# Performance work log

Hardware: AMD Instinct MI355X
Metric: run time of the kernel (lower is better)

Reference implementation:

```python
import jax, jax.numpy as jnp
import numpy as np

V, E, H = 32000, 256, 512
B, L = 32, 128
SOS = 0


def _lstm_cell(x, h, c, w_ih, w_hh, b_ih, b_hh):
    # PyTorch LSTMCell: gates ordered i, f, g, o
    gates = x @ w_ih.T + b_ih + h @ w_hh.T + b_hh  # (B, 4H)
    i, f, g, o = jnp.split(gates, 4, axis=-1)
    c_new = jax.nn.sigmoid(f) * c + jax.nn.sigmoid(i) * jnp.tanh(g)
    h_new = jax.nn.sigmoid(o) * jnp.tanh(c_new)
    return h_new, c_new


def setup_inputs() -> dict:
    key = jax.random.key(0)
    ks = jax.random.split(key, 14)
    s_e, s_h = 1.0 / np.sqrt(H), 1.0 / np.sqrt(H)
    return {
        "cnn_output": jax.random.normal(ks[0], (B, H), jnp.float32),
        "embedding": jax.random.normal(ks[1], (V, E), jnp.float32),
        "w_ih1": jax.random.uniform(ks[2], (4 * H, E), jnp.float32, -s_e, s_e),
        "w_hh1": jax.random.uniform(ks[3], (4 * H, H), jnp.float32, -s_e, s_e),
        "b_ih1": jax.random.uniform(ks[4], (4 * H,), jnp.float32, -s_e, s_e),
        "b_hh1": jax.random.uniform(ks[5], (4 * H,), jnp.float32, -s_e, s_e),
        "w_ih2": jax.random.uniform(ks[6], (4 * H, H), jnp.float32, -s_h, s_h),
        "w_hh2": jax.random.uniform(ks[7], (4 * H, H), jnp.float32, -s_h, s_h),
        "b_ih2": jax.random.uniform(ks[8], (4 * H,), jnp.float32, -s_h, s_h),
        "b_hh2": jax.random.uniform(ks[9], (4 * H,), jnp.float32, -s_h, s_h),
        "w_out": jax.random.uniform(ks[10], (V, H), jnp.float32, -s_h, s_h),
        "b_out": jax.random.uniform(ks[11], (V,), jnp.float32, -s_h, s_h),
        "ground_truth": jax.random.randint(ks[12], (B, L), 0, V, jnp.int64 if jax.config.jax_enable_x64 else jnp.int32),
    }


def reference(cnn_output, embedding, w_ih1, w_hh1, b_ih1, b_hh1,
              w_ih2, w_hh2, b_ih2, b_hh2, w_out, b_out, ground_truth):
    # Train mode, teacher_force = 1.0: input at step t is SOS for t=0 else ground_truth[:, t-1].
    batch = cnn_output.shape[0]
    tokens = jnp.concatenate(
        [jnp.full((batch, 1), SOS, ground_truth.dtype), ground_truth[:, :-1]], axis=1
    ).T  # (L, B)

    h1 = jnp.zeros_like(cnn_output)       # hidden_state = zeros
    c1 = cnn_output                        # cell_state   = cnn_output
    h2 = jnp.zeros_like(cnn_output)       # LSTMCell default zero state
    c2 = jnp.zeros_like(cnn_output)

    def step(carry, tok):
        h1, c1, h2, c2 = carry
        embed = embedding[tok]                                        # (B, E)
        h1, c1 = _lstm_cell(embed, h1, c1, w_ih1, w_hh1, b_ih1, b_hh1)
        h2, c2 = _lstm_cell(h1, h2, c2, w_ih2, w_hh2, b_ih2, b_hh2)
        logits = h2 @ w_out.T + b_out                                 # (B, V)
        logp = jax.nn.log_softmax(logits, axis=1)
        return (h1, c1, h2, c2), logp

    _, logps = jax.lax.scan(step, (h1, c1, h2, c2), tokens)  # (L, B, V)
    return jnp.transpose(logps, (1, 0, 2))  # (B, L, V) raw_pred_seq
```

## Files before the change

kernel.cpp:

```cpp
#include <hip/hip_runtime.h>
#include <hip/hip_bf16.h>
#include <stdint.h>

#define B_ 32
#define L_ 128
#define H_ 512
#define E_ 256
#define V_ 32000
#define G4 2048

typedef __attribute__((ext_vector_type(8))) short short8;
typedef __attribute__((ext_vector_type(4))) float f32x4;

__device__ __forceinline__ short f2bf(float f){
  uint32_t u = __builtin_bit_cast(uint32_t, f);
  u += 0x7FFFu + ((u >> 16) & 1u);
  return (short)(u >> 16);
}
__device__ __forceinline__ short8 ld8f_bf(const float* p){
  const f32x4* q = (const f32x4*)p;
  f32x4 a = q[0], b = q[1];
  short8 r;
  r[0]=f2bf(a[0]); r[1]=f2bf(a[1]); r[2]=f2bf(a[2]); r[3]=f2bf(a[3]);
  r[4]=f2bf(b[0]); r[5]=f2bf(b[1]); r[6]=f2bf(b[2]); r[7]=f2bf(b[3]);
  return r;
}
__device__ __forceinline__ f32x4 mfma16(short8 a, short8 b, f32x4 c){
  return __builtin_amdgcn_mfma_f32_16x16x32_bf16(a, b, c, 0, 0, 0);
}
__device__ __forceinline__ float sigm(float x){
  x = fminf(30.f, fmaxf(-30.f, x));
  return 1.f / (1.f + __expf(-x));
}
__device__ __forceinline__ float tanh_f(float x){
  x = fminf(15.f, fmaxf(-15.f, x));
  float e = __expf(-2.f * x);
  return (1.f - e) / (1.f + e);
}

__global__ void k_init(const float* __restrict__ cnn,
    const float* __restrict__ w_hh1, const float* __restrict__ w_ih2,
    const float* __restrict__ w_hh2,
    short* __restrict__ wb1, short* __restrict__ wb2, short* __restrict__ wb3,
    float* __restrict__ c1, float* __restrict__ c2, short* __restrict__ h1b,
    float* __restrict__ row_sum)
{
  const int stride = gridDim.x * blockDim.x;
  const int tid0 = blockIdx.x * blockDim.x + threadIdx.x;
  for (int i = tid0; i < G4 * H_; i += stride){
    wb1[i] = f2bf(w_hh1[i]); wb2[i] = f2bf(w_ih2[i]); wb3[i] = f2bf(w_hh2[i]);
  }
  for (int i = tid0; i < B_ * H_; i += stride){
    c1[i] = cnn[i]; c2[i] = 0.f; h1b[i] = 0; h1b[B_ * H_ + i] = 0;
  }
  for (int i = tid0; i < B_ * L_; i += stride) row_sum[i] = 0.f;
}

__global__ __launch_bounds__(256) void k_xw1(const int* __restrict__ gt,
    const float* __restrict__ emb, const float* __restrict__ w_ih1,
    const float* __restrict__ b_ih1, const float* __restrict__ b_hh1,
    float* __restrict__ xW1)
{
  const int wave = (blockIdx.x << 2) + (threadIdx.x >> 6);
  const int lane = threadIdx.x & 63, l15 = lane & 15, lg = lane >> 4;
  const int mt = wave >> 5, n0 = (wave & 31) * 64;
  const int r = mt * 16 + l15;
  const int tt = r >> 5, bb = r & 31;
  const int tok = (tt == 0) ? 0 : gt[bb * L_ + tt - 1];
  const float* arow = emb + (size_t)tok * E_ + lg * 8;

  f32x4 acc[4] = {};
  for (int kt = 0; kt < 8; ++kt){
    short8 af = ld8f_bf(arow + kt * 32);
    #pragma unroll
    for (int g = 0; g < 4; ++g){
      const int j = n0 + g * 16 + l15;
      short8 bw = ld8f_bf(w_ih1 + (size_t)j * E_ + kt * 32 + lg * 8);
      acc[g] = mfma16(af, bw, acc[g]);
    }
  }
  #pragma unroll
  for (int g = 0; g < 4; ++g){
    const int j = n0 + g * 16 + l15;
    const float bias = b_ih1[j] + b_hh1[j];
    const int rr = mt * 16 + lg * 4;
    #pragma unroll
    for (int reg = 0; reg < 4; ++reg)
      xW1[(size_t)(rr + reg) * G4 + j] = acc[g][reg] + bias;
  }
}

__global__ __launch_bounds__(256) void k_step(int t,
    const float* __restrict__ xW1,
    const short* __restrict__ wb1, const short* __restrict__ wb2,
    const short* __restrict__ wb3,
    const float* __restrict__ b_ih2, const float* __restrict__ b_hh2,
    short* __restrict__ h1b, float* __restrict__ c1, float* __restrict__ c2,
    short* __restrict__ h2all)
{
  __shared__ f32x4 red[3 * 512];
  const int bid = blockIdx.x;
  const int w = threadIdx.x >> 6;
  const int lane = threadIdx.x & 63;
  const int l15 = lane & 15, lg = lane >> 4;

  f32x4 acc[4][2] = {};
  const bool is_l1 = (bid < 32);

  if (is_l1){
    if (t >= L_) return;
    const int u0 = bid * 16;
    const short* h1r = h1b + (size_t)(t & 1) * (B_ * H_);
    const int kbase = w * 128;
    #pragma unroll
    for (int ki = 0; ki < 4; ++ki){
      const int k0 = kbase + ki * 32 + lg * 8;
      short8 a0 = *(const short8*)(h1r + (size_t)l15 * H_ + k0);
      short8 a1 = *(const short8*)(h1r + (size_t)(l15 + 16) * H_ + k0);
      #pragma unroll
      for (int g = 0; g < 4; ++g){
        short8 bw = *(const short8*)(wb1 + (size_t)(g * H_ + u0 + l15) * H_ + k0);
        acc[g][0] = mfma16(a0, bw, acc[g][0]);
        acc[g][1] = mfma16(a1, bw, acc[g][1]);
      }
    }
  } else {
    if (t < 1) return;
    const int s = t - 1;
    const int u0 = (bid - 32) * 16;
    const short* A = nullptr; const short* W = nullptr;
    if (w < 2){ A = h1b + (size_t)(t & 1) * (B_ * H_); W = wb2; }
    else if (s >= 1){ A = h2all + (size_t)(s - 1) * (B_ * H_); W = wb3; }
    if (A){
      const int kbase = (w & 1) * 256;
      #pragma unroll
      for (int ki = 0; ki < 8; ++ki){
        const int k0 = kbase + ki * 32 + lg * 8;
        short8 a0 = *(const short8*)(A + (size_t)l15 * H_ + k0);
        short8 a1 = *(const short8*)(A + (size_t)(l15 + 16) * H_ + k0);
        #pragma unroll
        for (int g = 0; g < 4; ++g){
          short8 bw = *(const short8*)(W + (size_t)(g * H_ + u0 + l15) * H_ + k0);
          acc[g][0] = mfma16(a0, bw, acc[g][0]);
          acc[g][1] = mfma16(a1, bw, acc[g][1]);
        }
      }
    }
  }

  if (w > 0){
    #pragma unroll
    for (int g = 0; g < 4; ++g)
      #pragma unroll
      for (int mt = 0; mt < 2; ++mt)
        red[(w - 1) * 512 + (g * 2 + mt) * 64 + lane] = acc[g][mt];
  }
  __syncthreads();
  if (w != 0) return;
  #pragma unroll
  for (int g = 0; g < 4; ++g)
    #pragma unroll
    for (int mt = 0; mt < 2; ++mt){
      f32x4 v = acc[g][mt];
      v += red[0 * 512 + (g * 2 + mt) * 64 + lane];
      v += red[1 * 512 + (g * 2 + mt) * 64 + lane];
      v += red[2 * 512 + (g * 2 + mt) * 64 + lane];
      acc[g][mt] = v;
    }

  if (is_l1){
    const int u = bid * 16 + l15;
    #pragma unroll
    for (int mt = 0; mt < 2; ++mt)
      #pragma unroll
      for (int reg = 0; reg < 4; ++reg){
        const int bb = mt * 16 + lg * 4 + reg;
        const float* xr = xW1 + (size_t)(t * B_ + bb) * G4;
        float gi = acc[0][mt][reg] + xr[0 * H_ + u];
        float gf = acc[1][mt][reg] + xr[1 * H_ + u];
        float gg = acc[2][mt][reg] + xr[2 * H_ + u];
        float go = acc[3][mt][reg] + xr[3 * H_ + u];
        float co = c1[bb * H_ + u];
        float cn = sigm(gf) * co + sigm(gi) * tanh_f(gg);
        float h  = sigm(go) * tanh_f(cn);
        c1[bb * H_ + u] = cn;
        h1b[(size_t)((t + 1) & 1) * (B_ * H_) + bb * H_ + u] = f2bf(h);
      }
  } else {
    const int s = t - 1;
    const int u = (bid - 32) * 16 + l15;
    float bias[4];
    #pragma unroll
    for (int g = 0; g < 4; ++g) bias[g] = b_ih2[g * H_ + u] + b_hh2[g * H_ + u];
    #pragma unroll
    for (int mt = 0; mt < 2; ++mt)
      #pragma unroll
      for (int reg = 0; reg < 4; ++reg){
        const int bb = mt * 16 + lg * 4 + reg;
        float gi = acc[0][mt][reg] + bias[0];
        float gf = acc[1][mt][reg] + bias[1];
        float gg = acc[2][mt][reg] + bias[2];
        float go = acc[3][mt][reg] + bias[3];
        float co = c2[bb * H_ + u];
        float cn = sigm(gf) * co + sigm(gi) * tanh_f(gg);
        float h  = sigm(go) * tanh_f(cn);
        c2[bb * H_ + u] = cn;
        h2all[(size_t)(s * B_ + bb) * H_ + u] = f2bf(h);
      }
  }
}

__global__ __launch_bounds__(256) void k_gemm_out(
    const short* __restrict__ h2all, const float* __restrict__ w_out,
    const float* __restrict__ b_out, float* __restrict__ out,
    float* __restrict__ row_sum)
{
  __shared__ __align__(16) short As[128 * 40];
  __shared__ __align__(16) short Bs[128 * 40];
  const int r0 = blockIdx.x * 128, n0 = blockIdx.y * 128;
  const int tid = threadIdx.x;
  const int w = tid >> 6, lane = tid & 63, l15 = lane & 15, lg = lane >> 4;
  const int mrow0 = (w >> 1) * 64, ncol0 = (w & 1) * 64;

  f32x4 acc[4][4] = {};

  for (int kt = 0; kt < 16; ++kt){
    const int kg = kt * 32;
    #pragma unroll
    for (int ss = 0; ss < 2; ++ss){
      const int slot = tid + ss * 256;
      const int row = slot >> 2, k8 = (slot & 3) * 8;
      *(short8*)(As + row * 40 + k8) =
          *(const short8*)(h2all + (size_t)(r0 + row) * H_ + kg + k8);
      *(short8*)(Bs + row * 40 + k8) =
          ld8f_bf(w_out + (size_t)(n0 + row) * H_ + kg + k8);
    }
    __syncthreads();
    short8 af[4], bfr[4];
    #pragma unroll
    for (int i = 0; i < 4; ++i){
      af[i]  = *(const short8*)(As + (mrow0 + i * 16 + l15) * 40 + lg * 8);
      bfr[i] = *(const short8*)(Bs + (ncol0 + i * 16 + l15) * 40 + lg * 8);
    }
    #pragma unroll
    for (int mi = 0; mi < 4; ++mi)
      #pragma unroll
      for (int nj = 0; nj < 4; ++nj)
        acc[mi][nj] = mfma16(af[mi], bfr[nj], acc[mi][nj]);
    __syncthreads();
  }

  float bo[4];
  #pragma unroll
  for (int nj = 0; nj < 4; ++nj) bo[nj] = b_out[n0 + ncol0 + nj * 16 + l15];

  #pragma unroll
  for (int mi = 0; mi < 4; ++mi){
    #pragma unroll
    for (int reg = 0; reg < 4; ++reg){
      const int r = r0 + mrow0 + mi * 16 + lg * 4 + reg;
      const int tt = r >> 5, bb = r & 31;
      float* orow = out + ((size_t)bb * L_ + tt) * V_;
      float esum = 0.f;
      #pragma unroll
      for (int nj = 0; nj < 4; ++nj){
        float logit = acc[mi][nj][reg] + bo[nj];
        orow[n0 + ncol0 + nj * 16 + l15] = logit;
        esum += __expf(logit);
      }
      esum += __shfl_xor(esum, 1);
      esum += __shfl_xor(esum, 2);
      esum += __shfl_xor(esum, 4);
      esum += __shfl_xor(esum, 8);
      if (l15 == 0) atomicAdd(&row_sum[r], esum);
    }
  }
}

__global__ void k_lse(float* row_sum){
  int i = blockIdx.x * blockDim.x + threadIdx.x;
  if (i < B_ * L_) row_sum[i] = __logf(row_sum[i]);
}

__global__ void k_fix(float* __restrict__ out, const float* __restrict__ lse){
  const size_t stride = (size_t)gridDim.x * blockDim.x;
  const size_t nvec = (size_t)B_ * L_ * V_ / 4;
  for (size_t i = (size_t)blockIdx.x * blockDim.x + threadIdx.x; i < nvec; i += stride){
    const int orow = (int)(i / (V_ / 4));
    const int tt = orow & (L_ - 1), bb = orow >> 7;
    const float l = lse[tt * B_ + bb];
    f32x4 v = ((const f32x4*)out)[i];
    v[0] -= l; v[1] -= l; v[2] -= l; v[3] -= l;
    ((f32x4*)out)[i] = v;
  }
}

extern "C" void kernel_launch(void* const* d_in, const int* in_sizes, int n_in,
                              void* d_out, int out_size, void* d_ws, size_t ws_size,
                              hipStream_t stream)
{
  (void)in_sizes; (void)n_in; (void)out_size;
  const float* cnn   = (const float*)d_in[0];
  const float* emb   = (const float*)d_in[1];
  const float* w_ih1 = (const float*)d_in[2];
  const float* w_hh1 = (const float*)d_in[3];
  const float* b_ih1 = (const float*)d_in[4];
  const float* b_hh1 = (const float*)d_in[5];
  const float* w_ih2 = (const float*)d_in[6];
  const float* w_hh2 = (const float*)d_in[7];
  const float* b_ih2 = (const float*)d_in[8];
  const float* b_hh2 = (const float*)d_in[9];
  const float* w_out = (const float*)d_in[10];
  const float* b_out = (const float*)d_in[11];
  const int*   gt    = (const int*)d_in[12];
  float* out = (float*)d_out;

  char* p = (char*)d_ws;
  size_t off = 0;
  auto carve = [&](size_t bytes)->char* {
    char* q = p + off; off = (off + bytes + 255) & ~(size_t)255; return q;
  };
  short* wb1     = (short*)carve(2097152);
  short* wb2     = (short*)carve(2097152);
  short* wb3     = (short*)carve(2097152);
  short* h2all   = (short*)carve(4194304);
  short* h1b     = (short*)carve(65536);
  float* c1      = (float*)carve(65536);
  float* c2      = (float*)carve(65536);
  float* row_sum = (float*)carve(16384);
  float* xW1;
  if (ws_size >= off + 33554432ull + 256ull){
    xW1 = (float*)carve(33554432);
  } else {
    xW1 = out;
  }

  hipLaunchKernelGGL(k_init, dim3(1024), dim3(256), 0, stream,
                     cnn, w_hh1, w_ih2, w_hh2, wb1, wb2, wb3, c1, c2, h1b, row_sum);
  hipLaunchKernelGGL(k_xw1, dim3(2048), dim3(256), 0, stream,
                     gt, emb, w_ih1, b_ih1, b_hh1, xW1);
  for (int t = 0; t <= L_; ++t)
    hipLaunchKernelGGL(k_step, dim3(64), dim3(256), 0, stream,
                       t, xW1, wb1, wb2, wb3, b_ih2, b_hh2, h1b, c1, c2, h2all);
  hipLaunchKernelGGL(k_gemm_out, dim3(32, 250), dim3(256), 0, stream,
                     h2all, w_out, b_out, out, row_sum);
  hipLaunchKernelGGL(k_lse, dim3(16), dim3(256), 0, stream, row_sum);
  hipLaunchKernelGGL(k_fix, dim3(2048), dim3(256), 0, stream, out, row_sum);
}
```

Before: 2.399 ms.

## Fuse recurrent steps into persistent cooperative kernel with register-resident weights

Replaces the 129 per-step launches with one cooperative kernel that keeps each block's recurrent weight slices in registers and uses grid.sync between time steps. Cell states now stay in registers, and the h2 layout changes to batch-major so the output GEMM and fix pass index rows directly. The output projection weights are pre-converted to bf16 once, and the GEMM uses a K=64 tile with XOR-swizzled shared memory. The cost is grid-wide barriers and heavy register pressure from holding 32 short8 weight fragments per thread.

```diff
diff --git a/kernel.cpp b/kernel.cpp
--- a/kernel.cpp
+++ b/kernel.cpp
@@ -1,6 +1,9 @@
 #include <hip/hip_runtime.h>
 #include <hip/hip_bf16.h>
+#include <hip/hip_cooperative_groups.h>
 #include <stdint.h>
+
+namespace cg = cooperative_groups;
 
 #define B_ 32
 #define L_ 128
@@ -38,21 +41,16 @@
   return (1.f - e) / (1.f + e);
 }
 
-__global__ void k_init(const float* __restrict__ cnn,
-    const float* __restrict__ w_hh1, const float* __restrict__ w_ih2,
-    const float* __restrict__ w_hh2,
-    short* __restrict__ wb1, short* __restrict__ wb2, short* __restrict__ wb3,
-    float* __restrict__ c1, float* __restrict__ c2, short* __restrict__ h1b,
-    float* __restrict__ row_sum)
+__global__ void k_init(const float* __restrict__ wout, short* __restrict__ wob,
+                       short* __restrict__ h1buf, float* __restrict__ row_sum)
 {
   const int stride = gridDim.x * blockDim.x;
   const int tid0 = blockIdx.x * blockDim.x + threadIdx.x;
-  for (int i = tid0; i < G4 * H_; i += stride){
-    wb1[i] = f2bf(w_hh1[i]); wb2[i] = f2bf(w_ih2[i]); wb3[i] = f2bf(w_hh2[i]);
-  }
-  for (int i = tid0; i < B_ * H_; i += stride){
-    c1[i] = cnn[i]; c2[i] = 0.f; h1b[i] = 0; h1b[B_ * H_ + i] = 0;
-  }
+  if (wob){
+    for (int i = tid0; i < V_ * H_ / 8; i += stride)
+      *(short8*)(wob + (size_t)i * 8) = ld8f_bf(wout + (size_t)i * 8);
+  }
+  for (int i = tid0; i < 2 * B_ * H_; i += stride) h1buf[i] = 0;
   for (int i = tid0; i < B_ * L_; i += stride) row_sum[i] = 0.f;
 }
 
@@ -90,133 +88,128 @@
   }
 }
 
-__global__ __launch_bounds__(256) void k_step(int t,
+__global__ __launch_bounds__(256, 1) void k_rnn(
     const float* __restrict__ xW1,
-    const short* __restrict__ wb1, const short* __restrict__ wb2,
-    const short* __restrict__ wb3,
+    const float* __restrict__ w_hh1, const float* __restrict__ w_ih2,
+    const float* __restrict__ w_hh2,
     const float* __restrict__ b_ih2, const float* __restrict__ b_hh2,
-    short* __restrict__ h1b, float* __restrict__ c1, float* __restrict__ c2,
-    short* __restrict__ h2all)
-{
-  __shared__ f32x4 red[3 * 512];
+    const float* __restrict__ cnn,
+    short* __restrict__ h1buf, short* __restrict__ h2all)
+{
+  __shared__ float gx[4][32][18];
   const int bid = blockIdx.x;
+  const bool isL1 = (bid < 32);
+  const int u0 = (isL1 ? bid : bid - 32) * 16;
   const int w = threadIdx.x >> 6;
   const int lane = threadIdx.x & 63;
   const int l15 = lane & 15, lg = lane >> 4;
-
-  f32x4 acc[4][2] = {};
-  const bool is_l1 = (bid < 32);
-
-  if (is_l1){
-    if (t >= L_) return;
-    const int u0 = bid * 16;
-    const short* h1r = h1b + (size_t)(t & 1) * (B_ * H_);
-    const int kbase = w * 128;
-    #pragma unroll
-    for (int ki = 0; ki < 4; ++ki){
-      const int k0 = kbase + ki * 32 + lg * 8;
-      short8 a0 = *(const short8*)(h1r + (size_t)l15 * H_ + k0);
-      short8 a1 = *(const short8*)(h1r + (size_t)(l15 + 16) * H_ + k0);
-      #pragma unroll
-      for (int g = 0; g < 4; ++g){
-        short8 bw = *(const short8*)(wb1 + (size_t)(g * H_ + u0 + l15) * H_ + k0);
-        acc[g][0] = mfma16(a0, bw, acc[g][0]);
-        acc[g][1] = mfma16(a1, bw, acc[g][1]);
-      }
-    }
+  const int cb = threadIdx.x >> 4;
+  const int cu = threadIdx.x & 15;
+
+  short8 wA[16], wB[16];
+  {
+    const float* W0 = isL1 ? w_hh1 : w_ih2;
+    const float* b0 = W0 + ((size_t)(w * H_ + u0 + l15)) * H_ + lg * 8;
+    #pragma unroll
+    for (int kt = 0; kt < 16; ++kt) wA[kt] = ld8f_bf(b0 + kt * 32);
+    if (!isL1){
+      const float* b1 = w_hh2 + ((size_t)(w * H_ + u0 + l15)) * H_ + lg * 8;
+      #pragma unroll
+      for (int kt = 0; kt < 16; ++kt) wB[kt] = ld8f_bf(b1 + kt * 32);
+    } else {
+      #pragma unroll
+      for (int kt = 0; kt < 16; ++kt) wB[kt] = short8{0,0,0,0,0,0,0,0};
+    }
+  }
+
+  float c_a, c_b, bias2[4];
+  if (isL1){
+    c_a = cnn[cb * H_ + u0 + cu];
+    c_b = cnn[(cb + 16) * H_ + u0 + cu];
+    bias2[0]=bias2[1]=bias2[2]=bias2[3]=0.f;
   } else {
-    if (t < 1) return;
-    const int s = t - 1;
-    const int u0 = (bid - 32) * 16;
-    const short* A = nullptr; const short* W = nullptr;
-    if (w < 2){ A = h1b + (size_t)(t & 1) * (B_ * H_); W = wb2; }
-    else if (s >= 1){ A = h2all + (size_t)(s - 1) * (B_ * H_); W = wb3; }
-    if (A){
-      const int kbase = (w & 1) * 256;
-      #pragma unroll
-      for (int ki = 0; ki < 8; ++ki){
-        const int k0 = kbase + ki * 32 + lg * 8;
-        short8 a0 = *(const short8*)(A + (size_t)l15 * H_ + k0);
-        short8 a1 = *(const short8*)(A + (size_t)(l15 + 16) * H_ + k0);
+    c_a = 0.f; c_b = 0.f;
+    #pragma unroll
+    for (int g = 0; g < 4; ++g)
+      bias2[g] = b_ih2[g * H_ + u0 + cu] + b_hh2[g * H_ + u0 + cu];
+  }
+
+  cg::grid_group grid = cg::this_grid();
+
+  for (int it = 0; it <= L_; ++it){
+    if (isL1 ? (it < L_) : (it >= 1)){
+      const int s = isL1 ? it : it - 1;
+      const short* h1r = h1buf + ((it + 1) & 1) * (B_ * H_);
+      float add_a[4] = {0.f,0.f,0.f,0.f}, add_b[4] = {0.f,0.f,0.f,0.f};
+      if (isL1){
+        const float* xr = xW1 + ((size_t)(s * B_ + cb)) * G4 + u0 + cu;
         #pragma unroll
         for (int g = 0; g < 4; ++g){
-          short8 bw = *(const short8*)(W + (size_t)(g * H_ + u0 + l15) * H_ + k0);
-          acc[g][0] = mfma16(a0, bw, acc[g][0]);
-          acc[g][1] = mfma16(a1, bw, acc[g][1]);
+          add_a[g] = xr[(size_t)g * H_];
+          add_b[g] = xr[(size_t)g * H_ + (size_t)16 * G4];
         }
-      }
-    }
-  }
-
-  if (w > 0){
-    #pragma unroll
-    for (int g = 0; g < 4; ++g)
-      #pragma unroll
-      for (int mt = 0; mt < 2; ++mt)
-        red[(w - 1) * 512 + (g * 2 + mt) * 64 + lane] = acc[g][mt];
-  }
-  __syncthreads();
-  if (w != 0) return;
-  #pragma unroll
-  for (int g = 0; g < 4; ++g)
-    #pragma unroll
-    for (int mt = 0; mt < 2; ++mt){
-      f32x4 v = acc[g][mt];
-      v += red[0 * 512 + (g * 2 + mt) * 64 + lane];
-      v += red[1 * 512 + (g * 2 + mt) * 64 + lane];
-      v += red[2 * 512 + (g * 2 + mt) * 64 + lane];
-      acc[g][mt] = v;
-    }
-
-  if (is_l1){
-    const int u = bid * 16 + l15;
-    #pragma unroll
-    for (int mt = 0; mt < 2; ++mt)
-      #pragma unroll
-      for (int reg = 0; reg < 4; ++reg){
-        const int bb = mt * 16 + lg * 4 + reg;
-        const float* xr = xW1 + (size_t)(t * B_ + bb) * G4;
-        float gi = acc[0][mt][reg] + xr[0 * H_ + u];
-        float gf = acc[1][mt][reg] + xr[1 * H_ + u];
-        float gg = acc[2][mt][reg] + xr[2 * H_ + u];
-        float go = acc[3][mt][reg] + xr[3 * H_ + u];
-        float co = c1[bb * H_ + u];
-        float cn = sigm(gf) * co + sigm(gi) * tanh_f(gg);
-        float h  = sigm(go) * tanh_f(cn);
-        c1[bb * H_ + u] = cn;
-        h1b[(size_t)((t + 1) & 1) * (B_ * H_) + bb * H_ + u] = f2bf(h);
-      }
-  } else {
-    const int s = t - 1;
-    const int u = (bid - 32) * 16 + l15;
-    float bias[4];
-    #pragma unroll
-    for (int g = 0; g < 4; ++g) bias[g] = b_ih2[g * H_ + u] + b_hh2[g * H_ + u];
-    #pragma unroll
-    for (int mt = 0; mt < 2; ++mt)
-      #pragma unroll
-      for (int reg = 0; reg < 4; ++reg){
-        const int bb = mt * 16 + lg * 4 + reg;
-        float gi = acc[0][mt][reg] + bias[0];
-        float gf = acc[1][mt][reg] + bias[1];
-        float gg = acc[2][mt][reg] + bias[2];
-        float go = acc[3][mt][reg] + bias[3];
-        float co = c2[bb * H_ + u];
-        float cn = sigm(gf) * co + sigm(gi) * tanh_f(gg);
-        float h  = sigm(go) * tanh_f(cn);
-        c2[bb * H_ + u] = cn;
-        h2all[(size_t)(s * B_ + bb) * H_ + u] = f2bf(h);
-      }
-  }
-}
-
+      } else {
+        #pragma unroll
+        for (int g = 0; g < 4; ++g){ add_a[g] = bias2[g]; add_b[g] = bias2[g]; }
+      }
+
+      f32x4 acc0 = {0.f,0.f,0.f,0.f}, acc1 = {0.f,0.f,0.f,0.f};
+      #pragma unroll
+      for (int kt = 0; kt < 16; ++kt){
+        const int k0 = kt * 32 + lg * 8;
+        short8 a0 = *(const short8*)(h1r + l15 * H_ + k0);
+        short8 a1 = *(const short8*)(h1r + (l15 + 16) * H_ + k0);
+        acc0 = mfma16(a0, wA[kt], acc0);
+        acc1 = mfma16(a1, wA[kt], acc1);
+      }
+      if (!isL1 && s >= 1){
+        const short* h2r = h2all + (size_t)(s - 1) * H_;
+        #pragma unroll
+        for (int kt = 0; kt < 16; ++kt){
+          const int k0 = kt * 32 + lg * 8;
+          short8 a0 = *(const short8*)(h2r + (size_t)l15 * (L_ * H_) + k0);
+          short8 a1 = *(const short8*)(h2r + (size_t)(l15 + 16) * (L_ * H_) + k0);
+          acc0 = mfma16(a0, wB[kt], acc0);
+          acc1 = mfma16(a1, wB[kt], acc1);
+        }
+      }
+      #pragma unroll
+      for (int r = 0; r < 4; ++r){
+        gx[w][lg * 4 + r][l15]      = acc0[r];
+        gx[w][lg * 4 + r + 16][l15] = acc1[r];
+      }
+      __syncthreads();
+      float ga[4], gb[4];
+      #pragma unroll
+      for (int g = 0; g < 4; ++g){
+        ga[g] = gx[g][cb][cu]      + add_a[g];
+        gb[g] = gx[g][cb + 16][cu] + add_b[g];
+      }
+      c_a = sigm(ga[1]) * c_a + sigm(ga[0]) * tanh_f(ga[2]);
+      float ha = sigm(ga[3]) * tanh_f(c_a);
+      c_b = sigm(gb[1]) * c_b + sigm(gb[0]) * tanh_f(gb[2]);
+      float hb = sigm(gb[3]) * tanh_f(c_b);
+      if (isL1){
+        short* h1w = h1buf + (it & 1) * (B_ * H_);
+        h1w[cb * H_ + u0 + cu]        = f2bf(ha);
+        h1w[(cb + 16) * H_ + u0 + cu] = f2bf(hb);
+      } else {
+        h2all[((size_t)cb * L_ + s) * H_ + u0 + cu]        = f2bf(ha);
+        h2all[((size_t)(cb + 16) * L_ + s) * H_ + u0 + cu] = f2bf(hb);
+      }
+    }
+    grid.sync();
+  }
+}
+
+template<bool PRE>
 __global__ __launch_bounds__(256) void k_gemm_out(
-    const short* __restrict__ h2all, const float* __restrict__ w_out,
-    const float* __restrict__ b_out, float* __restrict__ out,
-    float* __restrict__ row_sum)
-{
-  __shared__ __align__(16) short As[128 * 40];
-  __shared__ __align__(16) short Bs[128 * 40];
+    const short* __restrict__ h2all, const short* __restrict__ wob,
+    const float* __restrict__ wout, const float* __restrict__ b_out,
+    float* __restrict__ out, float* __restrict__ row_sum)
+{
+  __shared__ __align__(16) short As[128 * 64];
+  __shared__ __align__(16) short Bs[128 * 64];
   const int r0 = blockIdx.x * 128, n0 = blockIdx.y * 128;
   const int tid = threadIdx.x;
   const int w = tid >> 6, lane = tid & 63, l15 = lane & 15, lg = lane >> 4;
@@ -224,29 +217,39 @@
 
   f32x4 acc[4][4] = {};
 
-  for (int kt = 0; kt < 16; ++kt){
-    const int kg = kt * 32;
-    #pragma unroll
-    for (int ss = 0; ss < 2; ++ss){
-      const int slot = tid + ss * 256;
-      const int row = slot >> 2, k8 = (slot & 3) * 8;
-      *(short8*)(As + row * 40 + k8) =
-          *(const short8*)(h2all + (size_t)(r0 + row) * H_ + kg + k8);
-      *(short8*)(Bs + row * 40 + k8) =
-          ld8f_bf(w_out + (size_t)(n0 + row) * H_ + kg + k8);
+  for (int kt = 0; kt < 8; ++kt){
+    const int kg = kt * 64;
+    #pragma unroll
+    for (int i = 0; i < 4; ++i){
+      const int id = i * 256 + tid;
+      const int row = id >> 3, c = id & 7;
+      const int cs = c ^ (row & 7);
+      *(short8*)(As + row * 64 + cs * 8) =
+          *(const short8*)(h2all + (size_t)(r0 + row) * H_ + kg + c * 8);
+      if (PRE)
+        *(short8*)(Bs + row * 64 + cs * 8) =
+            *(const short8*)(wob + (size_t)(n0 + row) * H_ + kg + c * 8);
+      else
+        *(short8*)(Bs + row * 64 + cs * 8) =
+            ld8f_bf(wout + (size_t)(n0 + row) * H_ + kg + c * 8);
     }
     __syncthreads();
-    short8 af[4], bfr[4];
-    #pragma unroll
-    for (int i = 0; i < 4; ++i){
-      af[i]  = *(const short8*)(As + (mrow0 + i * 16 + l15) * 40 + lg * 8);
-      bfr[i] = *(const short8*)(Bs + (ncol0 + i * 16 + l15) * 40 + lg * 8);
-    }
-    #pragma unroll
-    for (int mi = 0; mi < 4; ++mi)
-      #pragma unroll
-      for (int nj = 0; nj < 4; ++nj)
-        acc[mi][nj] = mfma16(af[mi], bfr[nj], acc[mi][nj]);
+    #pragma unroll
+    for (int ks = 0; ks < 2; ++ks){
+      short8 af[4], bfr[4];
+      #pragma unroll
+      for (int i = 0; i < 4; ++i){
+        const int ra = mrow0 + i * 16 + l15;
+        af[i]  = *(const short8*)(As + ra * 64 + (((ks * 4 + lg) ^ (ra & 7)) * 8));
+        const int rb = ncol0 + i * 16 + l15;
+        bfr[i] = *(const short8*)(Bs + rb * 64 + (((ks * 4 + lg) ^ (rb & 7)) * 8));
+      }
+      #pragma unroll
+      for (int mi = 0; mi < 4; ++mi)
+        #pragma unroll
+        for (int nj = 0; nj < 4; ++nj)
+          acc[mi][nj] = mfma16(af[mi], bfr[nj], acc[mi][nj]);
+    }
     __syncthreads();
   }
 
@@ -259,8 +262,7 @@
     #pragma unroll
     for (int reg = 0; reg < 4; ++reg){
       const int r = r0 + mrow0 + mi * 16 + lg * 4 + reg;
-      const int tt = r >> 5, bb = r & 31;
-      float* orow = out + ((size_t)bb * L_ + tt) * V_;
+      float* orow = out + (size_t)r * V_;
       float esum = 0.f;
       #pragma unroll
       for (int nj = 0; nj < 4; ++nj){
@@ -287,8 +289,7 @@
   const size_t nvec = (size_t)B_ * L_ * V_ / 4;
   for (size_t i = (size_t)blockIdx.x * blockDim.x + threadIdx.x; i < nvec; i += stride){
     const int orow = (int)(i / (V_ / 4));
-    const int tt = orow & (L_ - 1), bb = orow >> 7;
-    const float l = lse[tt * B_ + bb];
+    const float l = lse[orow];
     f32x4 v = ((const f32x4*)out)[i];
     v[0] -= l; v[1] -= l; v[2] -= l; v[3] -= l;
     ((f32x4*)out)[i] = v;
@@ -320,30 +321,38 @@
   auto carve = [&](size_t bytes)->char* {
     char* q = p + off; off = (off + bytes + 255) & ~(size_t)255; return q;
   };
-  short* wb1     = (short*)carve(2097152);
-  short* wb2     = (short*)carve(2097152);
-  short* wb3     = (short*)carve(2097152);
-  short* h2all   = (short*)carve(4194304);
-  short* h1b     = (short*)carve(65536);
-  float* c1      = (float*)carve(65536);
-  float* c2      = (float*)carve(65536);
-  float* row_sum = (float*)carve(16384);
-  float* xW1;
-  if (ws_size >= off + 33554432ull + 256ull){
-    xW1 = (float*)carve(33554432);
-  } else {
-    xW1 = out;
-  }
-
-  hipLaunchKernelGGL(k_init, dim3(1024), dim3(256), 0, stream,
-                     cnn, w_hh1, w_ih2, w_hh2, wb1, wb2, wb3, c1, c2, h1b, row_sum);
+  short* h2all = (short*)carve(4194304);
+  short* h1buf = (short*)carve(65536);
+  float* lse   = (float*)carve(16384);
+  short* wob   = nullptr;
+  float* xW1   = (float*)out;
+  if (ws_size >= off + 33554432ull + 256ull) wob = (short*)carve(33554432);
+  if (ws_size >= off + 33554432ull + 256ull) xW1 = (float*)carve(33554432);
+
+  hipLaunchKernelGGL(k_init, dim3(2048), dim3(256), 0, stream, w_out, wob, h1buf, lse);
   hipLaunchKernelGGL(k_xw1, dim3(2048), dim3(256), 0, stream,
                      gt, emb, w_ih1, b_ih1, b_hh1, xW1);
-  for (int t = 0; t <= L_; ++t)
-    hipLaunchKernelGGL(k_step, dim3(64), dim3(256), 0, stream,
-                       t, xW1, wb1, wb2, wb3, b_ih2, b_hh2, h1b, c1, c2, h2all);
-  hipLaunchKernelGGL(k_gemm_out, dim3(32, 250), dim3(256), 0, stream,
-                     h2all, w_out, b_out, out, row_sum);
-  hipLaunchKernelGGL(k_lse, dim3(16), dim3(256), 0, stream, row_sum);
-  hipLaunchKernelGGL(k_fix, dim3(2048), dim3(256), 0, stream, out, row_sum);
-}
+
+  const float* xW1c = xW1;
+  void* args[9];
+  args[0] = (void*)&xW1c;
+  args[1] = (void*)&w_hh1;
+  args[2] = (void*)&w_ih2;
+  args[3] = (void*)&w_hh2;
+  args[4] = (void*)&b_ih2;
+  args[5] = (void*)&b_hh2;
+  args[6] = (void*)&cnn;
+  args[7] = (void*)&h1buf;
+  args[8] = (void*)&h2all;
+  hipLaunchCooperativeKernel(reinterpret_cast<void*>(k_rnn), dim3(64), dim3(256),
+                             args, 0, stream);
+
+  if (wob)
+    hipLaunchKernelGGL(HIP_KERNEL_NAME(k_gemm_out<true>), dim3(32, 250), dim3(256), 0, stream,
+                       h2all, wob, w_out, b_out, out, lse);
+  else
+    hipLaunchKernelGGL(HIP_KERNEL_NAME(k_gemm_out<false>), dim3(32, 250), dim3(256), 0, stream,
+                       h2all, wob, w_out, b_out, out, lse);
+  hipLaunchKernelGGL(k_lse, dim3(16), dim3(256), 0, stream, lse);
+  hipLaunchKernelGGL(k_fix, dim3(2048), dim3(256), 0, stream, out, lse);
+}
```

Result: slower. 3.050 ms (+27.2%).
